# Performance work log

Hardware: AMD Instinct MI355X
Metric: run time of the kernel (lower is better)

The kernel has to match this reference:

```python
import jax, jax.numpy as jnp
import numpy as np

D_K = 64  # per-head key dim, used for 1/sqrt(d_k) scaling


def setup_inputs() -> dict:
    key = jax.random.key(0)
    ks = jax.random.split(key, 9)
    B, S, D, H, DK, DV = 2, 4096, 512, 8, 64, 64
    s = 0.02
    return {
        "x": jax.random.normal(ks[0], (B, S, D), dtype=jnp.float32),
        "Wq": jax.random.normal(ks[1], (H, D, DK), dtype=jnp.float32) * s,
        "bq": jax.random.normal(ks[2], (H, DK), dtype=jnp.float32) * s,
        "Wk": jax.random.normal(ks[3], (H, D, DK), dtype=jnp.float32) * s,
        "bk": jax.random.normal(ks[4], (H, DK), dtype=jnp.float32) * s,
        "Wv": jax.random.normal(ks[5], (H, D, DV), dtype=jnp.float32) * s,
        "bv": jax.random.normal(ks[6], (H, DV), dtype=jnp.float32) * s,
        "Wo": jax.random.normal(ks[7], (H * DV, D), dtype=jnp.float32) * s,
        "bo": jax.random.normal(ks[8], (D,), dtype=jnp.float32) * s,
    }


def reference(x, Wq, bq, Wk, bk, Wv, bv, Wo, bo):
    # Per-head projections, vectorized over heads: [B,H,S,dk/dv]
    q = jnp.einsum("bsd,hdk->bhsk", x, Wq) + bq[None, :, None, :]
    k = jnp.einsum("bsd,hdk->bhsk", x, Wk) + bk[None, :, None, :]
    v = jnp.einsum("bsd,hdv->bhsv", x, Wv) + bv[None, :, None, :]
    # Scaled dot-product attention (no mask; dropout inactive at eval)
    scores = jnp.einsum("bhsk,bhtk->bhst", q, k) / jnp.sqrt(jnp.float32(D_K))
    attn = jax.nn.softmax(scores, axis=-1)
    o = jnp.einsum("bhst,bhtv->bhsv", attn, v)
    # Concat heads along feature dim: [B,S,H*dv]
    B, H, S, DV = o.shape
    concat = jnp.transpose(o, (0, 2, 1, 3)).reshape(B, S, H * DV)
    return concat @ Wo + bo
```

## Files before the change

### kernel.cpp

```cpp
#include <hip/hip_runtime.h>
#include <hip/hip_bf16.h>

typedef __attribute__((ext_vector_type(8))) short bf16x8;
typedef __attribute__((ext_vector_type(4))) float f32x4;
typedef __attribute__((ext_vector_type(16))) float f32x16;
typedef __attribute__((ext_vector_type(4))) unsigned short u16x4;
typedef __attribute__((ext_vector_type(4))) unsigned int u32x4;

#define NB 2
#define NS 4096
#define ND 512
#define NH 8

__device__ __forceinline__ unsigned short f2bf(float f) {
  unsigned int u = __float_as_uint(f);
  u += 0x7fffu + ((u >> 16) & 1u);
  return (unsigned short)(u >> 16);
}

__device__ __forceinline__ float bf2f(unsigned short h) {
  return __uint_as_float(((unsigned)h) << 16);
}

__device__ __forceinline__ float exp2_hw(float x) {
  float r;
  asm("v_exp_f32 %0, %1" : "=v"(r) : "v"(x));
  return r;
}

__device__ __forceinline__ unsigned cvtpk(float lo, float hi) {
  unsigned r;
  asm("v_cvt_pk_bf16_f32 %0, %1, %2" : "=v"(r) : "v"(lo), "v"(hi));
  return r;
}

__device__ __forceinline__ void swap32(unsigned& a, unsigned& b) {
  asm("v_permlane32_swap_b32 %0, %1" : "+v"(a), "+v"(b));
}

__device__ __forceinline__ bf16x8 mkfrag(unsigned w0, unsigned w1,
                                         unsigned w2, unsigned w3) {
  u32x4 u = {w0, w1, w2, w3};
  return __builtin_bit_cast(bf16x8, u);
}

__device__ __forceinline__ void gload_lds16(const unsigned short* g,
                                            unsigned short* l) {
  __builtin_amdgcn_global_load_lds(
      (const __attribute__((address_space(1))) unsigned int*)g,
      (__attribute__((address_space(3))) unsigned int*)l, 16, 0, 0);
}

__global__ void pack_kernel(const float* __restrict__ x,
                            const float* __restrict__ Wq,
                            const float* __restrict__ Wk,
                            const float* __restrict__ Wv,
                            const float* __restrict__ Wo,
                            unsigned short* __restrict__ x_bf,
                            unsigned short* __restrict__ w3,
                            unsigned short* __restrict__ wo_t)
{
  int idx = blockIdx.x * 256 + threadIdx.x;
  const int NX4 = NB * NS * ND / 4;
  const int NW = 512 * 512;
  if (idx < NX4) {
    const float4 f = ((const float4*)x)[idx];
    u16x4 o;
    o[0] = f2bf(f.x); o[1] = f2bf(f.y); o[2] = f2bf(f.z); o[3] = f2bf(f.w);
    ((u16x4*)x_bf)[idx] = o;
  } else if (idx < NX4 + 3 * NW) {
    int j = idx - NX4;
    int p = j / NW;
    int r = j - p * NW;
    int n = r >> 9, d = r & 511;
    int h = n >> 6, o = n & 63;
    const float* W = (p == 0) ? Wq : (p == 1) ? Wk : Wv;
    w3[j] = f2bf(W[(h * 512 + d) * 64 + o]);
  } else if (idx < NX4 + 4 * NW) {
    int j = idx - NX4 - 3 * NW;
    int n = j >> 9, kk = j & 511;
    wo_t[j] = f2bf(Wo[kk * 512 + n]);
  }
}

template <int MODE>
__global__ void gemm_bt(const unsigned short* __restrict__ A,
                        const unsigned short* __restrict__ Bm,
                        const float* __restrict__ b0,
                        const float* __restrict__ b1,
                        const float* __restrict__ b2,
                        unsigned short* __restrict__ qo,
                        unsigned short* __restrict__ ko,
                        unsigned short* __restrict__ vo,
                        float* __restrict__ fo) {
  __shared__ unsigned short Al[128 * 32];
  __shared__ unsigned short Bl[128 * 32];
  const int t = threadIdx.x;
  const int m0 = blockIdx.x * 128;
  const int n0 = blockIdx.y * 128;
  const int lane = t & 63;
  const int w = t >> 6;
  const int wm = w >> 1, wn = w & 1;
  const int c = lane & 15, g = lane >> 4;

  f32x4 acc[4][4];
#pragma unroll
  for (int i = 0; i < 4; ++i)
#pragma unroll
    for (int j = 0; j < 4; ++j) acc[i][j] = (f32x4){0.f, 0.f, 0.f, 0.f};

  const int srow = t >> 1, sseg = (t & 1) * 16;
  const unsigned short* Ap = A + (size_t)(m0 + srow) * 512 + sseg;
  const unsigned short* Bp = Bm + (size_t)(n0 + srow) * 512 + sseg;
  unsigned short* Alp = &Al[srow * 32 + sseg];
  unsigned short* Blp = &Bl[srow * 32 + sseg];

  for (int k0 = 0; k0 < 512; k0 += 32) {
    bf16x8 ra0 = *(const bf16x8*)(Ap + k0);
    bf16x8 ra1 = *(const bf16x8*)(Ap + k0 + 8);
    bf16x8 rb0 = *(const bf16x8*)(Bp + k0);
    bf16x8 rb1 = *(const bf16x8*)(Bp + k0 + 8);
    __syncthreads();
    *(bf16x8*)(Alp) = ra0;
    *(bf16x8*)(Alp + 8) = ra1;
    *(bf16x8*)(Blp) = rb0;
    *(bf16x8*)(Blp + 8) = rb1;
    __syncthreads();
    bf16x8 af[4], bfr[4];
#pragma unroll
    for (int mf = 0; mf < 4; ++mf)
      af[mf] = *(const bf16x8*)&Al[(wm * 64 + mf * 16 + c) * 32 + g * 8];
#pragma unroll
    for (int nf = 0; nf < 4; ++nf)
      bfr[nf] = *(const bf16x8*)&Bl[(wn * 64 + nf * 16 + c) * 32 + g * 8];
#pragma unroll
    for (int mf = 0; mf < 4; ++mf)
#pragma unroll
      for (int nf = 0; nf < 4; ++nf)
        acc[mf][nf] = __builtin_amdgcn_mfma_f32_16x16x32_bf16(
            af[mf], bfr[nf], acc[mf][nf], 0, 0, 0);
  }

  if (MODE == 0) {
    const int proj = n0 >> 9;
    const float* bias = proj == 0 ? b0 : (proj == 1 ? b1 : b2);
    unsigned short* dst01 = proj == 0 ? qo : ko;
    const float scale = proj == 0 ? 0.18033688011112042f : 1.0f;
#pragma unroll
    for (int nf = 0; nf < 4; ++nf) {
      const int col5 = (n0 + wn * 64 + nf * 16 + c) & 511;
      const int h = col5 >> 6, o = col5 & 63;
      const float bb = bias[col5];
#pragma unroll
      for (int mf = 0; mf < 4; ++mf) {
#pragma unroll
        for (int r = 0; r < 4; ++r) {
          const int m = m0 + wm * 64 + mf * 16 + g * 4 + r;
          const int b = m >> 12, s = m & 4095;
          const unsigned short hb = f2bf((acc[mf][nf][r] + bb) * scale);
          if (proj < 2)
            dst01[((size_t)((b * NH + h) * NS + s)) * 64 + o] = hb;
          else
            vo[((size_t)((b * NH + h) * 64 + o)) * NS + s] = hb;
        }
      }
    }
  } else {
#pragma unroll
    for (int nf = 0; nf < 4; ++nf) {
      const int col = n0 + wn * 64 + nf * 16 + c;
      const float bb = b0[col];
#pragma unroll
      for (int mf = 0; mf < 4; ++mf) {
#pragma unroll
        for (int r = 0; r < 4; ++r) {
          const int m = m0 + wm * 64 + mf * 16 + g * 4 + r;
          fo[(size_t)m * 512 + col] = acc[mf][nf][r] + bb;
        }
      }
    }
  }
}

template <int SPLITS>
__global__ __launch_bounds__(256, 2) void attn_kernel(
    const unsigned short* __restrict__ q,
    const unsigned short* __restrict__ k,
    const unsigned short* __restrict__ vt,
    unsigned short* __restrict__ cc,
    unsigned short* __restrict__ op,
    float* __restrict__ ml)
{
  union SMemU {
    struct { unsigned short Kl[2][4096]; unsigned short Vl[2][4096]; } kv;
    unsigned short Ol[4][32][68];
  };
  __shared__ SMemU sm;
  const int t = threadIdx.x;
  const int w = t >> 6, lane = t & 63;
  const int col = lane & 31, hi = lane >> 5;
  const int bh = blockIdx.y & 15;
  const int sp = blockIdx.y >> 4;
  const int b = bh >> 3, h = bh & 7;
  const int q0 = blockIdx.x * 128 + w * 32;
  const int kbase = sp * (NS / SPLITS);

  const unsigned short* qh = q + (size_t)bh * NS * 64;
  const unsigned short* kh = k + (size_t)bh * NS * 64;
  const unsigned short* vh = vt + (size_t)bh * 64 * NS;

  bf16x8 qf[4];
#pragma unroll
  for (int c = 0; c < 4; ++c)
    qf[c] = *(const bf16x8*)&qh[(size_t)(q0 + col) * 64 + c * 16 + hi * 8];

  const int rl = lane >> 3, chn = lane & 7;
  const int lk = rl * 64 + ((chn ^ (rl & 7)) << 3);
  const int lv = rl * NS + ((chn ^ (rl & 7)) << 3);

  auto ISSUE = [&](int tile, int bi) {
    const unsigned short* gk = kh + (size_t)(kbase + tile * 64 + w * 16) * 64;
    const unsigned short* gv = vh + (size_t)(w * 16) * NS + kbase + tile * 64;
    gload_lds16(gk + lk, &sm.kv.Kl[bi][w * 1024]);
    gload_lds16(gk + lk + 512, &sm.kv.Kl[bi][w * 1024 + 512]);
    gload_lds16(gv + lv, &sm.kv.Vl[bi][w * 1024]);
    gload_lds16(gv + lv + 8 * NS, &sm.kv.Vl[bi][w * 1024 + 512]);
  };

  f32x16 ot0, ot1;
#pragma unroll
  for (int r = 0; r < 16; ++r) { ot0[r] = 0.f; ot1[r] = 0.f; }
  float l_ = 0.f;

  const int NT = NS / (64 * SPLITS);

  ISSUE(0, 0);

  for (int it = 0; it < NT; ++it) {
    const int cur = it & 1;
    asm volatile("s_waitcnt vmcnt(0)" ::: "memory");
    __builtin_amdgcn_s_barrier();
    __builtin_amdgcn_sched_barrier(0);
    if (it + 1 < NT) ISSUE(it + 1, cur ^ 1);

    bf16x8 kfr[2][4];
#pragma unroll
    for (int c = 0; c < 4; ++c) {
      const int cidx = (((2 * c + hi) ^ (col & 7)) << 3);
      kfr[0][c] = *(const bf16x8*)&sm.kv.Kl[cur][col * 64 + cidx];
      kfr[1][c] = *(const bf16x8*)&sm.kv.Kl[cur][(col + 32) * 64 + cidx];
    }
    f32x16 p0, p1;
#pragma unroll
    for (int r = 0; r < 16; ++r) { p0[r] = 0.f; p1[r] = 0.f; }
    __builtin_amdgcn_s_setprio(1);
#pragma unroll
    for (int c = 0; c < 4; ++c) {
      p0 = __builtin_amdgcn_mfma_f32_32x32x16_bf16(kfr[0][c], qf[c], p0, 0, 0, 0);
      p1 = __builtin_amdgcn_mfma_f32_32x32x16_bf16(kfr[1][c], qf[c], p1, 0, 0, 0);
    }
    __builtin_amdgcn_s_setprio(0);

    bf16x8 vfr[2][4];
#pragma unroll
    for (int ks = 0; ks < 4; ++ks) {
      const int cidx = (((2 * ks + hi) ^ (col & 7)) << 3);
      vfr[0][ks] = *(const bf16x8*)&sm.kv.Vl[cur][col * 64 + cidx];
      vfr[1][ks] = *(const bf16x8*)&sm.kv.Vl[cur][(col + 32) * 64 + cidx];
    }

#pragma unroll
    for (int r = 0; r < 16; ++r) {
      p0[r] = exp2_hw(p0[r]);
      p1[r] = exp2_hw(p1[r]);
    }
    {
      float s[8];
#pragma unroll
      for (int r = 0; r < 8; ++r)
        s[r] = (p0[r] + p0[r + 8]) + (p1[r] + p1[r + 8]);
      float rs =
          ((s[0] + s[1]) + (s[2] + s[3])) + ((s[4] + s[5]) + (s[6] + s[7]));
      rs += __shfl_xor(rs, 32, 64);
      l_ += rs;
    }
    bf16x8 pb[4];
    {
      unsigned g0[8], g1[8];
#pragma unroll
      for (int gg = 0; gg < 8; ++gg) {
        g0[gg] = cvtpk(p0[2 * gg], p0[2 * gg + 1]);
        g1[gg] = cvtpk(p1[2 * gg], p1[2 * gg + 1]);
      }
      unsigned a1, b1, c1, d1;
      a1 = g0[0]; b1 = g0[2]; swap32(a1, b1);
      c1 = g0[1]; d1 = g0[3]; swap32(c1, d1);
      pb[0] = mkfrag(a1, c1, b1, d1);
      a1 = g0[4]; b1 = g0[6]; swap32(a1, b1);
      c1 = g0[5]; d1 = g0[7]; swap32(c1, d1);
      pb[1] = mkfrag(a1, c1, b1, d1);
      a1 = g1[0]; b1 = g1[2]; swap32(a1, b1);
      c1 = g1[1]; d1 = g1[3]; swap32(c1, d1);
      pb[2] = mkfrag(a1, c1, b1, d1);
      a1 = g1[4]; b1 = g1[6]; swap32(a1, b1);
      c1 = g1[5]; d1 = g1[7]; swap32(c1, d1);
      pb[3] = mkfrag(a1, c1, b1, d1);
    }

    __builtin_amdgcn_s_setprio(1);
#pragma unroll
    for (int ks = 0; ks < 4; ++ks) {
      ot0 = __builtin_amdgcn_mfma_f32_32x32x16_bf16(vfr[0][ks], pb[ks], ot0, 0, 0, 0);
      ot1 = __builtin_amdgcn_mfma_f32_32x32x16_bf16(vfr[1][ks], pb[ks], ot1, 0, 0, 0);
    }
    __builtin_amdgcn_s_setprio(0);
  }

  __syncthreads();

  const float inv = (SPLITS == 1) ? (1.0f / l_) : 1.0f;
#pragma unroll
  for (int r = 0; r < 16; ++r) {
    const int dvb = (r & 3) + 8 * (r >> 2) + 4 * hi;
    sm.Ol[w][col][dvb] = f2bf(ot0[r] * inv);
    sm.Ol[w][col][dvb + 32] = f2bf(ot1[r] * inv);
  }
  if (SPLITS > 1 && hi == 0)
    ml[(size_t)(sp * 16 + bh) * NS + q0 + col] = l_;
  asm volatile("s_waitcnt lgkmcnt(0)" ::: "memory");
  const int row = lane >> 1;
#pragma unroll
  for (int p = 0; p < 4; ++p) {
    const int chunk = (lane & 1) + 2 * p;
    bf16x8 vv = *(const bf16x8*)&sm.Ol[w][row][chunk * 8];
    if (SPLITS == 1)
      *(bf16x8*)&cc[((size_t)(b * NS + q0 + row)) * 512 + h * 64 + chunk * 8] =
          vv;
    else
      *(bf16x8*)&op[((size_t)(sp * 16 + bh) * NS + q0 + row) * 64 + chunk * 8] =
          vv;
  }
}

template <int SPLITS>
__global__ void combine_kernel(const unsigned short* __restrict__ op,
                               const float* __restrict__ ml,
                               unsigned short* __restrict__ cc) {
  const int id = blockIdx.x * 256 + threadIdx.x;
  const int chunk = id & 7;
  const int qq = (id >> 3) & 4095;
  const int bh = id >> 15;
  const int b = bh >> 3, h = bh & 7;
  float lsum = 0.f;
#pragma unroll
  for (int sp = 0; sp < SPLITS; ++sp)
    lsum += ml[(size_t)(sp * 16 + bh) * NS + qq];
  const float invl = 1.0f / lsum;
  float acc[8];
#pragma unroll
  for (int j = 0; j < 8; ++j) acc[j] = 0.f;
#pragma unroll
  for (int sp = 0; sp < SPLITS; ++sp) {
    const bf16x8 o =
        *(const bf16x8*)&op[((size_t)(sp * 16 + bh) * NS + qq) * 64 + chunk * 8];
#pragma unroll
    for (int j = 0; j < 8; ++j) acc[j] += bf2f((unsigned short)o[j]);
  }
  bf16x8 out;
#pragma unroll
  for (int j = 0; j < 8; ++j) out[j] = (short)f2bf(acc[j] * invl);
  *(bf16x8*)&cc[((size_t)(b * NS + qq)) * 512 + h * 64 + chunk * 8] = out;
}

extern "C" void kernel_launch(void* const* d_in, const int* in_sizes, int n_in,
                              void* d_out, int out_size, void* d_ws, size_t ws_size,
                              hipStream_t stream) {
  const float* x  = (const float*)d_in[0];
  const float* Wq = (const float*)d_in[1];
  const float* bq = (const float*)d_in[2];
  const float* Wk = (const float*)d_in[3];
  const float* bk = (const float*)d_in[4];
  const float* Wv = (const float*)d_in[5];
  const float* bv = (const float*)d_in[6];
  const float* Wo = (const float*)d_in[7];
  const float* bo = (const float*)d_in[8];

  unsigned char* ws = (unsigned char*)d_ws;
  unsigned short* x_bf = (unsigned short*)(ws);
  unsigned short* w3   = (unsigned short*)(ws + 8388608);
  unsigned short* wo_t = (unsigned short*)(ws + 9961472);
  unsigned short* qb   = (unsigned short*)(ws + 10485760);
  unsigned short* kb   = (unsigned short*)(ws + 18874368);
  unsigned short* vb   = (unsigned short*)(ws + 27262976);
  unsigned short* op   = (unsigned short*)(ws + 35651584);
  unsigned short* cc   = x_bf;

  const size_t need2 = 35651584ull + 2ull * 8388608 + 2ull * 16 * 4096 * 4;

  pack_kernel<<<8192, 256, 0, stream>>>(x, Wq, Wk, Wv, Wo, x_bf, w3, wo_t);
  gemm_bt<0><<<dim3(64, 12), 256, 0, stream>>>(x_bf, w3, bq, bk, bv, qb, kb, vb,
                                               nullptr);
  if (ws_size >= need2) {
    float* mlp = (float*)(ws + 35651584 + 2ull * 8388608);
    attn_kernel<2><<<dim3(32, 32), 256, 0, stream>>>(qb, kb, vb, nullptr, op,
                                                     mlp);
    combine_kernel<2><<<2048, 256, 0, stream>>>(op, mlp, cc);
  } else {
    attn_kernel<1><<<dim3(32, 16), 256, 0, stream>>>(qb, kb, vb, cc, nullptr,
                                                     nullptr);
  }
  gemm_bt<1><<<dim3(64, 4), 256, 0, stream>>>(cc, wo_t, bo, nullptr, nullptr,
                                              nullptr, nullptr, nullptr,
                                              (float*)d_out);
}
```

Measured before the change: 145.9 us.

## Double-buffer GEMM via direct global-to-LDS loads and split attention KV four ways

The projection GEMM now uses two LDS buffers filled by direct global-to-LDS loads, so the next K-slice loads while MFMAs run on the current one. It also raises wave priority around the MFMA block and sets launch bounds to allow two blocks per CU. When the workspace is large enough, attention splits the key/value sequence into four parts instead of two, giving more blocks, with a combine pass merging the partial results. The four-way split costs more partial-output traffic and combine work, and the double buffer doubles LDS use per block.

```diff
diff --git a/kernel.cpp b/kernel.cpp
--- a/kernel.cpp
+++ b/kernel.cpp
@@ -84,17 +84,18 @@
 }
 
 template <int MODE>
-__global__ void gemm_bt(const unsigned short* __restrict__ A,
-                        const unsigned short* __restrict__ Bm,
-                        const float* __restrict__ b0,
-                        const float* __restrict__ b1,
-                        const float* __restrict__ b2,
-                        unsigned short* __restrict__ qo,
-                        unsigned short* __restrict__ ko,
-                        unsigned short* __restrict__ vo,
-                        float* __restrict__ fo) {
-  __shared__ unsigned short Al[128 * 32];
-  __shared__ unsigned short Bl[128 * 32];
+__global__ __launch_bounds__(256, 2) void gemm_bt(
+    const unsigned short* __restrict__ A,
+    const unsigned short* __restrict__ Bm,
+    const float* __restrict__ b0,
+    const float* __restrict__ b1,
+    const float* __restrict__ b2,
+    unsigned short* __restrict__ qo,
+    unsigned short* __restrict__ ko,
+    unsigned short* __restrict__ vo,
+    float* __restrict__ fo) {
+  __shared__ unsigned short Al[2][128 * 32];
+  __shared__ unsigned short Bl[2][128 * 32];
   const int t = threadIdx.x;
   const int m0 = blockIdx.x * 128;
   const int n0 = blockIdx.y * 128;
@@ -109,36 +110,42 @@
 #pragma unroll
     for (int j = 0; j < 4; ++j) acc[i][j] = (f32x4){0.f, 0.f, 0.f, 0.f};
 
-  const int srow = t >> 1, sseg = (t & 1) * 16;
-  const unsigned short* Ap = A + (size_t)(m0 + srow) * 512 + sseg;
-  const unsigned short* Bp = Bm + (size_t)(n0 + srow) * 512 + sseg;
-  unsigned short* Alp = &Al[srow * 32 + sseg];
-  unsigned short* Blp = &Bl[srow * 32 + sseg];
-
-  for (int k0 = 0; k0 < 512; k0 += 32) {
-    bf16x8 ra0 = *(const bf16x8*)(Ap + k0);
-    bf16x8 ra1 = *(const bf16x8*)(Ap + k0 + 8);
-    bf16x8 rb0 = *(const bf16x8*)(Bp + k0);
-    bf16x8 rb1 = *(const bf16x8*)(Bp + k0 + 8);
-    __syncthreads();
-    *(bf16x8*)(Alp) = ra0;
-    *(bf16x8*)(Alp + 8) = ra1;
-    *(bf16x8*)(Blp) = rb0;
-    *(bf16x8*)(Blp + 8) = rb1;
-    __syncthreads();
+  const int rr = lane >> 2;
+  const int kc = (lane & 3) * 8;
+  const unsigned short* Ab = A + (size_t)(m0 + w * 32 + rr) * 512 + kc;
+  const unsigned short* Bb = Bm + (size_t)(n0 + w * 32 + rr) * 512 + kc;
+
+  auto ISSUE = [&](int ks, int bi) {
+    const int k0 = ks * 32;
+    gload_lds16(Ab + k0, &Al[bi][w * 1024]);
+    gload_lds16(Ab + 16 * 512 + k0, &Al[bi][w * 1024 + 512]);
+    gload_lds16(Bb + k0, &Bl[bi][w * 1024]);
+    gload_lds16(Bb + 16 * 512 + k0, &Bl[bi][w * 1024 + 512]);
+  };
+
+  ISSUE(0, 0);
+  for (int ks = 0; ks < 16; ++ks) {
+    const int cur = ks & 1;
+    asm volatile("s_waitcnt vmcnt(0)" ::: "memory");
+    __builtin_amdgcn_s_barrier();
+    __builtin_amdgcn_sched_barrier(0);
+    if (ks + 1 < 16) ISSUE(ks + 1, cur ^ 1);
+
     bf16x8 af[4], bfr[4];
 #pragma unroll
     for (int mf = 0; mf < 4; ++mf)
-      af[mf] = *(const bf16x8*)&Al[(wm * 64 + mf * 16 + c) * 32 + g * 8];
+      af[mf] = *(const bf16x8*)&Al[cur][(wm * 64 + mf * 16 + c) * 32 + g * 8];
 #pragma unroll
     for (int nf = 0; nf < 4; ++nf)
-      bfr[nf] = *(const bf16x8*)&Bl[(wn * 64 + nf * 16 + c) * 32 + g * 8];
+      bfr[nf] = *(const bf16x8*)&Bl[cur][(wn * 64 + nf * 16 + c) * 32 + g * 8];
+    __builtin_amdgcn_s_setprio(1);
 #pragma unroll
     for (int mf = 0; mf < 4; ++mf)
 #pragma unroll
       for (int nf = 0; nf < 4; ++nf)
         acc[mf][nf] = __builtin_amdgcn_mfma_f32_16x16x32_bf16(
             af[mf], bfr[nf], acc[mf][nf], 0, 0, 0);
+    __builtin_amdgcn_s_setprio(0);
   }
 
   if (MODE == 0) {
@@ -395,12 +402,18 @@
   unsigned short* op   = (unsigned short*)(ws + 35651584);
   unsigned short* cc   = x_bf;
 
+  const size_t need4 = 35651584ull + 4ull * 8388608 + 4ull * 16 * 4096 * 4;
   const size_t need2 = 35651584ull + 2ull * 8388608 + 2ull * 16 * 4096 * 4;
 
   pack_kernel<<<8192, 256, 0, stream>>>(x, Wq, Wk, Wv, Wo, x_bf, w3, wo_t);
   gemm_bt<0><<<dim3(64, 12), 256, 0, stream>>>(x_bf, w3, bq, bk, bv, qb, kb, vb,
                                                nullptr);
-  if (ws_size >= need2) {
+  if (ws_size >= need4) {
+    float* mlp = (float*)(ws + 35651584 + 4ull * 8388608);
+    attn_kernel<4><<<dim3(32, 64), 256, 0, stream>>>(qb, kb, vb, nullptr, op,
+                                                     mlp);
+    combine_kernel<4><<<2048, 256, 0, stream>>>(op, mlp, cc);
+  } else if (ws_size >= need2) {
     float* mlp = (float*)(ws + 35651584 + 2ull * 8388608);
     attn_kernel<2><<<dim3(32, 32), 256, 0, stream>>>(qb, kb, vb, nullptr, op,
                                                      mlp);
```

Result: no change. 144.5 us (-0.9%).
